# Performance work log

Hardware: AMD Instinct MI355X
Metric: run time of the kernel (lower is better)

The kernel has to match this reference:

```python
import jax, jax.numpy as jnp
import numpy as np

NE = 32          # n_events
S = 65536        # n_samples
FR = 128         # n_frames
SR = 22050       # samplerate
NRES = 1024      # n_resonances
IEXP = 8         # instr_expressivity
NEXP = 4         # noise_expressivity
NFILT = 64       # n_noise_filters
FSAMP = 512      # noise_filter_samples
NDEF = 64        # n_deformations
NNDEF = 32       # noise_deformations
NENV = 64        # n_envelopes
NDEC = 64        # n_decays
ENV_SMALL = 128  # Envelopes n_samples
ENV_FULL = 8192  # Envelopes full_size
NVERB = 16       # number of impulse responses


def interp_last(x, size):
    # linear interpolation along last axis (align_corners=True style)
    n = x.shape[-1]
    pos = jnp.linspace(0.0, n - 1.0, size)
    lo = jnp.floor(pos).astype(jnp.int32)
    hi = jnp.clip(lo + 1, 0, n - 1)
    w = (pos - lo).astype(x.dtype)
    return x[..., lo] * (1.0 - w) + x[..., hi] * w


def fft_convolve(a, b):
    # linear convolution via zero-padded FFT, keep first n samples
    n = a.shape[-1]
    A = jnp.fft.rfft(a, n=2 * n)
    B = jnp.fft.rfft(b, n=2 * n)
    return jnp.fft.irfft(A * B, n=2 * n)[..., :n]


def select_items(sel, items):
    # softmax-weighted soft lookup over item bank
    return jax.nn.softmax(sel, axis=-1) @ items


def make_waves(n_samples, n_res, sr):
    freqs = np.linspace(20.0, 4000.0, num=n_res // 4)
    t = np.arange(n_samples, dtype=np.float64) / sr
    ph = freqs[:, None] * t[None, :]               # cycles
    sine = np.sin(2 * np.pi * ph)
    saw = 2.0 * (ph % 1.0) - 1.0
    square = np.sign(sine)
    tri = 2.0 * np.abs(saw) - 1.0
    w = np.concatenate([sine, saw, square, tri], axis=0)  # (n_res, n_samples)
    return jnp.asarray(w, dtype=jnp.float32)


def setup_inputs() -> dict:
    key = jax.random.key(0)
    ks = jax.random.split(key, 16)
    u = lambda k, shp: jax.random.uniform(k, shp, minval=-0.02, maxval=0.02, dtype=jnp.float32)
    inp = {
        'res_sel': jax.random.normal(ks[0], (1, NE, IEXP, NRES), jnp.float32),
        'noise_sel': jax.random.normal(ks[1], (1, NE, NEXP, NFILT), jnp.float32),
        'env_sel': jax.random.normal(ks[2], (1, NE, NENV), jnp.float32),
        'dec_sel': jax.random.normal(ks[3], (1, NE, 1, NDEC), jnp.float32),
        'def_sel': jax.random.normal(ks[4], (1, NE, NDEF), jnp.float32),
        'noise_def_sel': jax.random.normal(ks[5], (1, NE, NNDEF), jnp.float32),
        'mix_sel': jax.random.normal(ks[6], (1, NE, 2), jnp.float32),
        'room_sel': jax.random.normal(ks[7], (1, NE, NVERB), jnp.float32),
        'amp': jax.random.uniform(ks[8], (1, NE, 1), dtype=jnp.float32),
        # learned item banks (uniform(-0.02, 0.02) init as in Lookup)
        'r_items': u(ks[9], (NRES, NRES)),
        'n_items': u(ks[10], (NFILT, FSAMP)),
        'e_items': u(ks[11], (NENV, ENV_SMALL)),
        'd_items': u(ks[12], (NDEC, 1)),
        'warp_items': u(ks[13], (NDEF, IEXP * FR)),
        'nwarp_items': u(ks[14], (NNDEF, NEXP * FR)),
        # fixed buffers
        'verbs': jax.random.normal(ks[15], (NVERB, S), jnp.float32) * 0.01,
        'waves': make_waves(S, NRES, SR),
    }
    return inp


def reference(res_sel, noise_sel, env_sel, dec_sel, def_sel, noise_def_sel,
              mix_sel, room_sel, amp, r_items, n_items, e_items, d_items,
              warp_items, nwarp_items, verbs, waves):
    # --- Envelopes: items**2, soft lookup, upsample, multiply by noise, pad ---
    env = select_items(env_sel, e_items ** 2)            # (1, NE, 128)
    env = interp_last(env, ENV_FULL)                     # (1, NE, 8192)
    noise = jax.random.uniform(jax.random.key(42), env.shape,
                               minval=-1.0, maxval=1.0, dtype=env.dtype)
    env = env * noise
    impulses = jnp.pad(env, ((0, 0), (0, 0), (0, S - ENV_FULL)))  # (1, NE, S)

    # --- SampleLookup (windowed noise filters) ---
    k = jnp.arange(FSAMP, dtype=jnp.float32)
    hamming = 0.54 - 0.46 * jnp.cos(2.0 * jnp.pi * k / (FSAMP - 1))
    nfil = select_items(noise_sel, n_items * hamming)    # (1, NE, NEXP, FSAMP)
    nfil = jnp.pad(nfil, ((0, 0), (0, 0), (0, 0), (0, S - FSAMP)))
    filt = fft_convolve(impulses[:, :, None, :], nfil)   # (1, NE, NEXP, S)

    # --- noise Deformations: softmax over channel dim, upsample ---
    nd = select_items(noise_def_sel, nwarp_items)        # (1, NE, NEXP*FR)
    nd = nd.reshape(1, NE, NEXP, FR)
    nd = jax.nn.softmax(nd, axis=2)
    nd = interp_last(nd, S)                              # (1, NE, NEXP, S)
    filtered = (filt * nd).sum(axis=2)                   # (1, NE, S)

    # --- WavetableLookup resonances ---
    res = select_items(res_sel, r_items) @ waves         # (1, NE, IEXP, S)

    # --- Decays: log-domain cumsum -> exponential envelopes ---
    d_pre = 0.5 + jax.nn.sigmoid(d_items) * 0.5          # base_resonance=0.5
    d = select_items(dec_sel, d_pre)                     # (1, NE, 1, 1)
    d = jnp.tile(d, (1, 1, 1, FR))                       # (1, NE, 1, FR)
    d = jnp.exp(jnp.cumsum(jnp.log(d + 1e-12), axis=-1))
    d = interp_last(d, S)                                # (1, NE, 1, S)

    # --- instrument Deformations ---
    w = select_items(def_sel, warp_items)                # (1, NE, IEXP*FR)
    w = w.reshape(1, NE, IEXP, FR)
    w = jax.nn.softmax(w, axis=2)
    w = interp_last(w, S)                                # (1, NE, IEXP, S)

    dres = (res * d * w).sum(axis=2)                     # (1, NE, S)

    # --- excite resonances with filtered noise, add reverb, mix ---
    conv = fft_convolve(filtered, dres)                  # (1, NE, S)
    rooms = select_items(room_sel, verbs)                # (1, NE, S)
    wet = fft_convolve(conv, rooms)
    m = jax.nn.softmax(mix_sel, axis=-1)                 # (1, NE, 2)
    mixed = m[..., 0:1] * conv + m[..., 1:2] * wet
    return mixed * (amp ** 2)                            # (1, NE, S)
```

## Files before the change

### kernel.cpp

```cpp
#include <hip/hip_runtime.h>
#include <math.h>

#define NEV    32
#define NS     65536
#define NFFT   131072
#define ENVS   128
#define ENVF   8192
#define FSAMP2 512
#define NEXP2  4
#define FLEN   8704
#define GD     5622750u
#define GDH    2811375u

enum : size_t {
  O_ENV_SMALL = 0,
  O_NFIL      = 4096,
  O_IMP       = 69632,
  O_ND        = 331776,
  O_WSM       = 348160,
  O_DSM       = 380928,
  O_SCAL      = 385024,
  O_RHO       = 385152,
  O_P1        = 385664,
  O_P2        = 647808,
// ... 73 lines not shown
  x0 += x1; x1 = tf_rotl(x1, 6); x1 ^= x0;
  x0 += k2; x1 += k0 + 5u;
  return x0 ^ x1;
}

__global__ __launch_bounds__(64) void weights_kernel(
    const float* __restrict__ noise_sel, const float* __restrict__ env_sel,
    const float* __restrict__ dec_sel,   const float* __restrict__ def_sel,
    const float* __restrict__ ndef_sel,  const float* __restrict__ mix_sel,
    const float* __restrict__ room_sel,  const float* __restrict__ amp,
    const float* __restrict__ d_items,
    float* __restrict__ swE, float* __restrict__ swN,
    float* __restrict__ swD, float* __restrict__ swND,
    float* __restrict__ d_small, float* __restrict__ scal,
    float* __restrict__ rho)
{
  const int e = blockIdx.x;
  const int l = threadIdx.x;

  {
    float x = env_sel[e*64 + l];
    float mx = wmax(x);
    float ex = expf(x - mx);
    float sm = wsum(ex);
    swE[e*64 + l] = ex / sm;
  }
  #pragma unroll
  for (int x4 = 0; x4 < NEXP2; x4++){
    float v = noise_sel[(e*NEXP2 + x4)*64 + l];
    float mxv = wmax(v);
    float exv = expf(v - mxv);
    float smv = wsum(exv);
    swN[(e*NEXP2 + x4)*64 + l] = exv / smv;
  }
  {
    float x = def_sel[e*64 + l];
    float mx = wmax(x);
    float ex = expf(x - mx);
    float sm = wsum(ex);
    swD[e*64 + l] = ex / sm;
  }
  {
    float x = (l < 32) ? ndef_sel[e*32 + l] : -1e30f;
    float mx = wmax(x);
    float ex = (l < 32) ? expf(x - mx) : 0.f;
    float sm = wsum(ex);
    if (l < 32) swND[e*32 + l] = ex / sm;
  }
  {
    float x = dec_sel[e*64 + l];
    float mx = wmax(x);
    float ex = expf(x - mx);
    float sm = wsum(ex);
    float wgt = ex / sm;
    float di = d_items[l];
    float dp = 0.5f + 0.5f*(1.0f/(1.0f + expf(-di)));
    float d0 = wsum(wgt*dp);
    float ld = logf(d0 + 1e-12f);
    #pragma unroll
    for (int c = 0; c < 2; c++){
      int f = l + 64*c;
      d_small[e*128 + f] = expf((float)(f+1)*ld);
    }
  }
  if (l == 0){
    float a = mix_sel[e*2 + 0], b = mix_sel[e*2 + 1];
    float mm = fmaxf(a, b);
    float ea = expf(a - mm), eb = expf(b - mm);
    float ss = ea + eb;
    scal[e*4 + 0] = ea/ss;
    scal[e*4 + 1] = eb/ss;
    float am = amp[e];
    scal[e*4 + 2] = am*am;
  }
  {
    float x = (l < 16) ? room_sel[e*16 + l] : -1e30f;
    float mx = wmax(x);
    float ex = (l < 16) ? expf(x - mx) : 0.f;
    float sm = wsum(ex);
    if (l < 16) rho[e*16 + l] = ex/sm;
  }
}

__global__ __launch_bounds__(128) void envs_kernel(
    const float* __restrict__ swE, const float* __restrict__ e_items,
    float* __restrict__ env_small)
{
  const int e = blockIdx.x, j = threadIdx.x;
  __shared__ float sw[64];
  if (j < 64) sw[j] = swE[e*64 + j];
  __syncthreads();
  float acc = 0.f;
  #pragma unroll 8
  for (int k = 0; k < 64; k++){ float it = e_items[k*ENVS + j]; acc += sw[k]*(it*it); }
  env_small[e*ENVS + j] = acc;
}

__global__ __launch_bounds__(256) void nfil_kernel(
    const float* __restrict__ swN, const float* __restrict__ n_items,
    float* __restrict__ nfil)
{
  const int b = blockIdx.x;
  const int tid = threadIdx.x;
  __shared__ float sw[64];
  if (tid < 64) sw[tid] = swN[b*64 + tid];
  __syncthreads();
  #pragma unroll
  for (int c = 0; c < 2; c++){
    int tau = tid + 256*c;
    float acc = 0.f;
    #pragma unroll 8
    for (int f = 0; f < 64; f++) acc += sw[f]*n_items[f*FSAMP2 + tau];
    float ham = 0.54f - 0.46f*cosf((6.2831853071795864769f * (float)tau) / 511.0f);
    nfil[b*FSAMP2 + tau] = acc*ham;
  }
}

__global__ __launch_bounds__(128) void warp_kernel(
    const float* __restrict__ swD, const float* __restrict__ warp_items,
    float* __restrict__ w_small)
{
  const int e = blockIdx.x, f = threadIdx.x;
  __shared__ float sw[64];
  if (f < 64) sw[f] = swD[e*64 + f];
  __syncthreads();
  float acc[8] = {0,0,0,0,0,0,0,0};
  for (int k = 0; k < 64; k++){
    float wk = sw[k];
    const float* row = warp_items + (size_t)k*1024 + f;
    #pragma unroll
    for (int i = 0; i < 8; i++) acc[i] += wk*row[i*128];
  }
  float mx = -1e30f;
  #pragma unroll
  for (int i = 0; i < 8; i++) mx = fmaxf(mx, acc[i]);
  float ev[8]; float s = 0.f;
  #pragma unroll
  for (int i = 0; i < 8; i++){ ev[i] = expf(acc[i] - mx); s += ev[i]; }
  #pragma unroll
  for (int i = 0; i < 8; i++) w_small[(e*8 + i)*128 + f] = ev[i]/s;
}

__global__ __launch_bounds__(128) void nwarp_kernel(
    const float* __restrict__ swND, const float* __restrict__ nwarp_items,
    float* __restrict__ nd_small)
{
  const int e = blockIdx.x, f = threadIdx.x;
  __shared__ float sw[32];
  if (f < 32) sw[f] = swND[e*32 + f];
  __syncthreads();
  float acc[4] = {0,0,0,0};
  for (int k = 0; k < 32; k++){
    float wk = sw[k];
    const float* row = nwarp_items + (size_t)k*512 + f;
    #pragma unroll
    for (int x = 0; x < 4; x++) acc[x] += wk*row[x*128];
  }
  float mx = -1e30f;
  #pragma unroll
  for (int x = 0; x < 4; x++) mx = fmaxf(mx, acc[x]);
  float ev[4]; float s = 0.f;
  #pragma unroll
  for (int x = 0; x < 4; x++){ ev[x] = expf(acc[x] - mx); s += ev[x]; }
  #pragma unroll
  for (int x = 0; x < 4; x++) nd_small[(e*4 + x)*128 + f] = ev[x]/s;
}

__global__ __launch_bounds__(64) void prep_kernel(
    const float* __restrict__ noise_sel, const float* __restrict__ env_sel,
    const float* __restrict__ dec_sel,   const float* __restrict__ def_sel,
    const float* __restrict__ ndef_sel,  const float* __restrict__ mix_sel,
    const float* __restrict__ room_sel,  const float* __restrict__ amp,
    const float* __restrict__ n_items,   const float* __restrict__ e_items,
    const float* __restrict__ d_items,   const float* __restrict__ warp_items,
    const float* __restrict__ nwarp_items,
    float* __restrict__ env_small, float* __restrict__ nfil,
    float* __restrict__ nd_small,  float* __restrict__ w_small,
    float* __restrict__ d_small,   float* __restrict__ scal,
    float* __restrict__ rho)
{
  const int e = blockIdx.x;
  const int l = threadIdx.x;
  __shared__ float sw[64];
  __shared__ float buf[1024];

  {
    float x = env_sel[e*64 + l];
    float mx = wmax(x);
    float ex = expf(x - mx);
    float sm = wsum(ex);
    sw[l] = ex / sm;
  }
  __syncthreads();
  #pragma unroll
  for (int c = 0; c < 2; c++){
    int j = l + 64*c;
    float acc = 0.f;
    for (int k = 0; k < 64; k++){ float it = e_items[k*ENVS + j]; acc += sw[k]*(it*it); }
    env_small[e*ENVS + j] = acc;
  }
  __syncthreads();

  for (int x = 0; x < NEXP2; x++){
    float v = noise_sel[(e*NEXP2 + x)*64 + l];
    float mxv = wmax(v);
    float exv = expf(v - mxv);
    float smv = wsum(exv);
    sw[l] = exv / smv;
    __syncthreads();
    for (int c = 0; c < 8; c++){
      int tau = l + 64*c;
      float acc = 0.f;
      for (int f = 0; f < 64; f++) acc += sw[f]*n_items[f*FSAMP2 + tau];
      float ham = 0.54f - 0.46f*cosf((6.2831853071795864769f * (float)tau) / 511.0f);
      nfil[(e*NEXP2 + x)*FSAMP2 + tau] = acc*ham;
    }
    __syncthreads();
  }

  {
    float x = def_sel[e*64 + l];
    float mx = wmax(x);
    float ex = expf(x - mx);
    float sm = wsum(ex);
    sw[l] = ex / sm;
  }
  __syncthreads();
  for (int c = 0; c < 16; c++){
    int idx = l + 64*c;
    float acc = 0.f;
    for (int k = 0; k < 64; k++) acc += sw[k]*warp_items[k*1024 + idx];
    buf[idx] = acc;
  }
  __syncthreads();
  #pragma unroll
  for (int c = 0; c < 2; c++){
    int f = l + 64*c;
    float mx = -1e30f;
    for (int i = 0; i < 8; i++) mx = fmaxf(mx, buf[i*128 + f]);
    float ev[8]; float s = 0.f;
    for (int i = 0; i < 8; i++){ ev[i] = expf(buf[i*128 + f] - mx); s += ev[i]; }
    for (int i = 0; i < 8; i++) w_small[(e*8 + i)*128 + f] = ev[i]/s;
  }
  __syncthreads();

  {
    float x = (l < 32) ? ndef_sel[e*32 + l] : -1e30f;
    float mx = wmax(x);
// ... 20 lines not shown
  }
  __syncthreads();

  {
    float x = dec_sel[e*64 + l];
    float mx = wmax(x);
    float ex = expf(x - mx);
    float sm = wsum(ex);
    float wgt = ex / sm;
    float di = d_items[l];
    float dp = 0.5f + 0.5f*(1.0f/(1.0f + expf(-di)));
    float d0 = wsum(wgt*dp);
    float ld = logf(d0 + 1e-12f);
    #pragma unroll
    for (int c = 0; c < 2; c++){
      int f = l + 64*c;
      d_small[e*128 + f] = expf((float)(f+1)*ld);
    }
  }
  if (l == 0){
    float a = mix_sel[e*2 + 0], b = mix_sel[e*2 + 1];
    float mm = fmaxf(a, b);
    float ea = expf(a - mm), eb = expf(b - mm);
    float ss = ea + eb;
    scal[e*4 + 0] = ea/ss;
    scal[e*4 + 1] = eb/ss;
    float am = amp[e];
    scal[e*4 + 2] = am*am;
  }
  {
    float x = (l < 16) ? room_sel[e*16 + l] : -1e30f;
    float mx = wmax(x);
    float ex = (l < 16) ? expf(x - mx) : 0.f;
    float sm = wsum(ex);
    if (l < 16) rho[e*16 + l] = ex/sm;
  }
}

__global__ __launch_bounds__(256) void p1_softmax_kernel(
    const float* __restrict__ res_sel, float* __restrict__ P1)
{
  const int m = blockIdx.x;
  const int tid = threadIdx.x;
  __shared__ float red[4], red2[4];
  const float* row = res_sel + (size_t)m*1024;
  float4 v = ((const float4*)row)[tid];
  float mx = fmaxf(fmaxf(v.x, v.y), fmaxf(v.z, v.w));
  #pragma unroll
  for (int o = 32; o > 0; o >>= 1) mx = fmaxf(mx, __shfl_xor(mx, o));
  if ((tid & 63) == 0) red[tid >> 6] = mx;
  __syncthreads();
  mx = fmaxf(fmaxf(red[0], red[1]), fmaxf(red[2], red[3]));
  float e0 = expf(v.x - mx), e1 = expf(v.y - mx), e2 = expf(v.z - mx), e3 = expf(v.w - mx);
  float s = e0 + e1 + e2 + e3;
  #pragma unroll
  for (int o = 32; o > 0; o >>= 1) s += __shfl_xor(s, o);
  if ((tid & 63) == 0) red2[tid >> 6] = s;
  __syncthreads();
  s = red2[0] + red2[1] + red2[2] + red2[3];
  float inv = 1.0f/s;
  ((float4*)(P1 + (size_t)m*1024))[tid] = make_float4(e0*inv, e1*inv, e2*inv, e3*inv);
}

__global__ __launch_bounds__(256) void p2_kernel(
    const float* __restrict__ P1, const float* __restrict__ r_items,
    float* __restrict__ P2)
{
  __shared__ __align__(16) float sp1[8][1024];
  const int bx = blockIdx.x;
  const int mg = blockIdx.y;
  const int tid = threadIdx.x;
  for (int idx = tid; idx < 2048; idx += 256)
    ((float4*)&sp1[0][0])[idx] = ((const float4*)(P1 + (size_t)mg*8*1024))[idx];
  __syncthreads();
  const int n = bx*256 + tid;
  float acc[8] = {0,0,0,0,0,0,0,0};
  for (int k = 0; k < 1024; k++){
    float wv = r_items[(size_t)k*1024 + n];
    #pragma unroll
    for (int r = 0; r < 8; r++) acc[r] += sp1[r][k]*wv;
  }
  #pragma unroll
  for (int r = 0; r < 8; r++) P2[(size_t)(mg*8 + r)*1024 + n] = acc[r];
}

__global__ __launch_bounds__(256) void split_a_kernel(
    const float* __restrict__ P2, unsigned short* __restrict__ Ahi)
{
  const int row = blockIdx.x;
  for (int k = threadIdx.x; k < 1024; k += 256){
    float f = P2[(size_t)row*1024 + k];
    Ahi[(size_t)(k >> 3)*2048 + row*8 + (k & 7)] = f2bf(f);
  }
}

__global__ __launch_bounds__(256) void env_noise_kernel(
    const float* __restrict__ env_small, float* __restrict__ impulses)
{
  const int flat = blockIdx.x*256 + threadIdx.x;
  const int e = flat >> 13, i = flat & 8191;
  unsigned bits = threefry_bits(0u, (unsigned)flat);
  float u01 = __uint_as_float((bits >> 9) | 0x3f800000u) - 1.0f;
  float nz  = fmaxf(-1.0f, u01*2.0f - 1.0f);
  float pos = (float)i * (127.0f/8191.0f);
  int lo = (int)floorf(pos);
  int hi = imin(lo + 1, 127);
  float w = pos - (float)lo;
  const float* es = env_small + e*ENVS;
  float v = es[lo]*(1.0f - w) + es[hi]*w;
  impulses[flat] = v*nz;
}

__global__ __launch_bounds__(256) void filt_kernel(
    const float* __restrict__ nfil, const float* __restrict__ impulses,
    const float* __restrict__ nd_small, float* __restrict__ filtered)
{
  __shared__ float nf[4*512];
  __shared__ float imp[768];
  const int e = blockIdx.y, t0 = blockIdx.x*256, tid = threadIdx.x;
  for (int idx = tid; idx < 2048; idx += 256) nf[idx] = nfil[e*2048 + idx];
  for (int idx = tid; idx < 768; idx += 256){
    int g = t0 - 512 + idx;
    imp[idx] = (g >= 0 && g < ENVF) ? impulses[e*ENVF + g] : 0.f;
  }
  __syncthreads();
  const int t = t0 + tid;
  float s0 = 0.f, s1 = 0.f, s2 = 0.f, s3 = 0.f;
  for (int tau = 0; tau < 512; tau++){
    float iv = imp[512 + tid - tau];
    s0 += nf[0*512 + tau]*iv;
    s1 += nf[1*512 + tau]*iv;
    s2 += nf[2*512 + tau]*iv;
    s3 += nf[3*512 + tau]*iv;
  }
  float pos = (float)t * (127.0f/65535.0f);
  int lo = (int)floorf(pos);
  int hi = imin(lo + 1, 127);
  float w = pos - (float)lo;
  const float* nds = nd_small + e*512;
  float acc = 0.f;
  acc += s0*(nds[0*128 + lo]*(1.0f - w) + nds[0*128 + hi]*w);
  acc += s1*(nds[1*128 + lo]*(1.0f - w) + nds[1*128 + hi]*w);
  acc += s2*(nds[2*128 + lo]*(1.0f - w) + nds[2*128 + hi]*w);
  acc += s3*(nds[3*128 + lo]*(1.0f - w) + nds[3*128 + hi]*w);
  filtered[e*FLEN + t] = acc;
}

__global__ __launch_bounds__(256) void rooms_kernel(
    const float* __restrict__ verbs, const float* __restrict__ rho,
    float* __restrict__ rooms)
{
  const int t = blockIdx.x*256 + threadIdx.x;
  const int e = blockIdx.y;
  float acc = 0.f;
  #pragma unroll
  for (int v = 0; v < 16; v++) acc += rho[e*16 + v]*verbs[(size_t)v*NS + t];
  rooms[(size_t)e*NS + t] = acc;
}

__device__ __noinline__ float slow_wave(int wf, int n, int i){
  const double stp = 3980.0 / 255.0;
  double fi = (i == 255) ? 4000.0 : __dadd_rn(__dmul_rn((double)i, stp), 20.0);
  double tn = (double)n / 22050.0;
  double ph = __dmul_rn(fi, tn);
  double fr = ph - trunc(ph);
  if (wf == 1) return (float)(2.0*fr - 1.0);
  if (wf == 3){ double sw = 2.0*fr - 1.0; return (float)(2.0*fabs(sw) - 1.0); }
  if (fr == 0.0 || fr == 0.5){
    if (ph == 0.0) return 0.0f;
    double sv = sin(__dmul_rn(6.283185307179586, ph));
    return (sv > 0.0) ? 1.0f : ((sv < 0.0) ? -1.0f : 0.0f);
  }
  return (fr < 0.5) ? 1.0f : -1.0f;
}

__device__ __forceinline__ void gen8(int wf, int n, int i0,
// ... 198 lines not shown
                                         float* __restrict__ yi)
{
  const int tid = threadIdx.x;
  constexpr int BPR = L/4;
  #pragma unroll
  for (int q = 0; q < 4; q++){
    int bf = tid + 256*q;
    int r  = bf / BPR;
    int j  = bf % BPR;
    int sw = (r & 7) << 2;
    int jm = j & (Ns - 1);
    float2 w1 = twid((float)jm * (1.0f/(4.0f*(float)Ns)));
    if (DIR < 0) w1.y = -w1.y;
    float2 w2 = make_float2(w1.x*w1.x - w1.y*w1.y, 2.0f*w1.x*w1.y);
    float2 w3 = make_float2(w2.x*w1.x - w2.y*w1.y, w2.x*w1.y + w2.y*w1.x);
    const float* xrr = xr + r*L;
    const float* xir = xi + r*L;
    float ar  = xrr[j ^ sw],           ai  = xir[j ^ sw];
    float b0r = xrr[(j+BPR) ^ sw],     b0i = xir[(j+BPR) ^ sw];
    float c0r = xrr[(j+2*BPR) ^ sw],   c0i = xir[(j+2*BPR) ^ sw];
    float d0r = xrr[(j+3*BPR) ^ sw],   d0i = xir[(j+3*BPR) ^ sw];
    float br = b0r*w1.x - b0i*w1.y,  bi = b0r*w1.y + b0i*w1.x;
    float cr = c0r*w2.x - c0i*w2.y,  ci = c0r*w2.y + c0i*w2.x;
    float dr = d0r*w3.x - d0i*w3.y,  di = d0r*w3.y + d0i*w3.x;
    float apc_r = ar + cr, apc_i = ai + ci;
    float amc_r = ar - cr, amc_i = ai - ci;
    float bpd_r = br + dr, bpd_i = bi + di;
    float bmd_r = br - dr, bmd_i = bi - di;
    int dbase = ((j - jm) << 2) + jm;
    float* yrr = yr + r*L;
    float* yir = yi + r*L;
    yrr[dbase ^ sw]          = apc_r + bpd_r;
    yir[dbase ^ sw]          = apc_i + bpd_i;
    yrr[(dbase + 2*Ns) ^ sw] = apc_r - bpd_r;
    yir[(dbase + 2*Ns) ^ sw] = apc_i - bpd_i;
    if (DIR > 0){
      yrr[(dbase + Ns) ^ sw]   = amc_r + bmd_i;
      yir[(dbase + Ns) ^ sw]   = amc_i - bmd_r;
      yrr[(dbase + 3*Ns) ^ sw] = amc_r - bmd_i;
      yir[(dbase + 3*Ns) ^ sw] = amc_i + bmd_r;
    } else {
      yrr[(dbase + Ns) ^ sw]   = amc_r - bmd_i;
      yir[(dbase + Ns) ^ sw]   = amc_i + bmd_r;
      yrr[(dbase + 3*Ns) ^ sw] = amc_r + bmd_i;
      yir[(dbase + 3*Ns) ^ sw] = amc_i - bmd_r;
    }
  }
}

#define FFT_SWAP { float* t_; t_=ra;ra=rb;rb=t_; t_=ia;ia=ib;ib=t_; }

template<int L, int DIR>
__device__ __forceinline__ void fft_core4(float*& ra, float*& ia, float*& rb, float*& ib)
{
  const int tid = threadIdx.x;
  if (L == 512){
    __syncthreads();
    #pragma unroll
    for (int q = 0; q < 8; q++){
      int bf = tid + 256*q;
      int r = bf >> 8, j = bf & 255;
      int sw = (r & 7) << 2;
      float ar = ra[r*512 + (j ^ sw)],        ai = ia[r*512 + (j ^ sw)];
      float br = ra[r*512 + ((j+256) ^ sw)],  bi = ia[r*512 + ((j+256) ^ sw)];
      rb[r*512 + ((2*j) ^ sw)]   = ar + br;
      ib[r*512 + ((2*j) ^ sw)]   = ai + bi;
      rb[r*512 + ((2*j+1) ^ sw)] = ar - br;
      ib[r*512 + ((2*j+1) ^ sw)] = ai - bi;
    }
    FFT_SWAP
    __syncthreads(); r4_stage<512,   2, DIR>(ra, ia, rb, ib); FFT_SWAP
    __syncthreads(); r4_stage<512,   8, DIR>(ra, ia, rb, ib); FFT_SWAP
    __syncthreads(); r4_stage<512,  32, DIR>(ra, ia, rb, ib); FFT_SWAP
    __syncthreads(); r4_stage<512, 128, DIR>(ra, ia, rb, ib); FFT_SWAP
  } else {
    __syncthreads(); r4_stage<256,   1, DIR>(ra, ia, rb, ib); FFT_SWAP
    __syncthreads(); r4_stage<256,   4, DIR>(ra, ia, rb, ib); FFT_SWAP
    __syncthreads(); r4_stage<256,  16, DIR>(ra, ia, rb, ib); FFT_SWAP
    __syncthreads(); r4_stage<256,  64, DIR>(ra, ia, rb, ib); FFT_SWAP
  }
  __syncthreads();
}

__global__ __launch_bounds__(256) void fwd512_pack_kernel(
    const float* __restrict__ srcA, int lenA, int strideA,
    const float* __restrict__ srcB, int lenB, int strideB,
    float2* __restrict__ Bt)
{
  __shared__ float reA[4096], imA[4096], reB[4096], imB[4096];
  const int e = blockIdx.y, t1 = blockIdx.x*8, tid = threadIdx.x;
  #pragma unroll
  for (int q = 0; q < 4; q++){
    int flat = tid + 256*q;
    int n2 = flat >> 1;
    int rb = (flat & 1)*4;
    int nb = t1 + rb + 256*n2;
    float4 va = make_float4(0.f,0.f,0.f,0.f);
    float4 vb = make_float4(0.f,0.f,0.f,0.f);
    if (nb < lenA) va = *(const float4*)(srcA + (size_t)e*strideA + nb);
    if (nb < lenB) vb = *(const float4*)(srcB + (size_t)e*strideB + nb);
    #pragma unroll
    for (int j = 0; j < 4; j++){
      int r = rb + j;
      int sw = (r & 7) << 2;
      reA[r*512 + (n2 ^ sw)] = (&va.x)[j];
      imA[r*512 + (n2 ^ sw)] = (&vb.x)[j];
    }
  }
  float *ra = reA, *ia = imA, *rb2 = reB, *ib2 = imB;
  fft_core4<512, +1>(ra, ia, rb2, ib2);
  float2* dst = Bt + ((size_t)e << 17);
  #pragma unroll
  for (int q = 0; q < 16; q++){
    int idx = tid + 256*q;
    int r = idx & 7, k2 = idx >> 3;
    int n1 = t1 + r;
    int sw = (r & 7) << 2;
    float xr = ra[r*512 + (k2 ^ sw)];
    float xi = ia[r*512 + (k2 ^ sw)];
    float2 w = twid((float)(n1*k2) * (1.0f/131072.0f));
    dst[k2*256 + n1] = make_float2(xr*w.x - xi*w.y, xr*w.y + xi*w.x);
  }
}

__global__ __launch_bounds__(256) void fwd512_pack_rooms_kernel(
    const float* __restrict__ verbs, const float* __restrict__ rho,
    float2* __restrict__ Bt)
{
  __shared__ float reA[4096], imA[4096], reB[4096], imB[4096];
  __shared__ float srho[32];
  const int e = blockIdx.y, t1 = blockIdx.x*8, tid = threadIdx.x;
  if (tid < 32) srho[tid] = rho[(2*e)*16 + tid];
  __syncthreads();
  #pragma unroll
  for (int q = 0; q < 4; q++){
    int flat = tid + 256*q;
    int n2 = flat >> 1;
    int rb = (flat & 1)*4;
    int nb = t1 + rb + 256*n2;
    float4 va = make_float4(0.f,0.f,0.f,0.f);
    float4 vb = make_float4(0.f,0.f,0.f,0.f);
    if (nb < NS){
      #pragma unroll
      for (int v = 0; v < 16; v++){
        float4 w4 = *(const float4*)(verbs + (size_t)v*NS + nb);
        float r0 = srho[v], r1 = srho[16 + v];
        va.x += r0*w4.x; va.y += r0*w4.y; va.z += r0*w4.z; va.w += r0*w4.w;
        vb.x += r1*w4.x; vb.y += r1*w4.y; vb.z += r1*w4.z; vb.w += r1*w4.w;
      }
    }
    #pragma unroll
    for (int j = 0; j < 4; j++){
      int r = rb + j;
      int sw = (r & 7) << 2;
      reA[r*512 + (n2 ^ sw)] = (&va.x)[j];
      imA[r*512 + (n2 ^ sw)] = (&vb.x)[j];
    }
  }
  float *ra = reA, *ia = imA, *rb2 = reB, *ib2 = imB;
  fft_core4<512, +1>(ra, ia, rb2, ib2);
  float2* dst = Bt + ((size_t)e << 17);
  #pragma unroll
  for (int q = 0; q < 16; q++){
    int idx = tid + 256*q;
    int r = idx & 7, k2 = idx >> 3;
    int n1 = t1 + r;
    int sw = (r & 7) << 2;
    float xr = ra[r*512 + (k2 ^ sw)];
    float xi = ia[r*512 + (k2 ^ sw)];
    float2 w = twid((float)(n1*k2) * (1.0f/131072.0f));
    dst[k2*256 + n1] = make_float2(xr*w.x - xi*w.y, xr*w.y + xi*w.x);
  }
}

__global__ __launch_bounds__(256) void fwd256_kernel(float2* __restrict__ S)
{
  __shared__ float reA[4096], imA[4096], reB[4096], imB[4096];
  const int e = blockIdx.y, K0 = blockIdx.x*16, tid = threadIdx.x;
  float2* base = S + ((size_t)e << 17) + (size_t)K0*256;
  #pragma unroll
  for (int q = 0; q < 16; q++){
    int idx = tid + 256*q;
    int r = idx >> 8, col = idx & 255;
    float2 v = base[r*256 + col];
    int sw = (r & 7) << 2;
    reA[r*256 + (col ^ sw)] = v.x;
    imA[r*256 + (col ^ sw)] = v.y;
  }
  float *ra = reA, *ia = imA, *rb = reB, *ib = imB;
  fft_core4<256, +1>(ra, ia, rb, ib);
  #pragma unroll
  for (int q = 0; q < 16; q++){
    int idx = tid + 256*q;
    int r = idx >> 8, col = idx & 255;
    int sw = (r & 7) << 2;
    base[r*256 + col] = make_float2(ra[r*256 + (col ^ sw)], ia[r*256 + (col ^ sw)]);
  }
}

__global__ __launch_bounds__(256) void inv256_mul2_kernel(
    const float2* __restrict__ ZA, const float2* __restrict__ ZB,
    float2* __restrict__ Ut)
{
  __shared__ float reA[4096], imA[4096], reB[4096], imB[4096];
  const int e = blockIdx.y, K0 = blockIdx.x*16, tid = threadIdx.x;
  const float2* Za = ZA + ((size_t)e << 17);
  const float2* Zb = ZB + ((size_t)e << 17);
  #pragma unroll
  for (int q = 0; q < 16; q++){
    int idx = tid + 256*q;
    int r = idx >> 8, col = idx & 255;
    int k2 = K0 + r;
    int k2p, k1p;
    if (k2 == 0){ k2p = 0; k1p = (256 - col) & 255; }
    else        { k2p = 512 - k2; k1p = 255 - col; }
    float2 za  = Za[(size_t)k2*256 + col];
    float2 zap = Za[(size_t)k2p*256 + k1p];
    float2 zb  = Zb[(size_t)k2*256 + col];
    float2 zbp = Zb[(size_t)k2p*256 + k1p];
    float a0r = 0.5f*(za.x + zap.x), a0i = 0.5f*(za.y - zap.y);
    float a1r = 0.5f*(za.y + zap.y), a1i = 0.5f*(zap.x - za.x);
    float b0r = 0.5f*(zb.x + zbp.x), b0i = 0.5f*(zb.y - zbp.y);
    float b1r = 0.5f*(zb.y + zbp.y), b1i = 0.5f*(zbp.x - zb.x);
    float p0r = a0r*b0r - a0i*b0i, p0i = a0r*b0i + a0i*b0r;
    float p1r = a1r*b1r - a1i*b1i, p1i = a1r*b1i + a1i*b1r;
    int sw = (r & 7) << 2;
    reA[r*256 + (col ^ sw)] = p0r - p1i;
    imA[r*256 + (col ^ sw)] = p0i + p1r;
  }
  float *ra = reA, *ia = imA, *rb = reB, *ib = imB;
  fft_core4<256, -1>(ra, ia, rb, ib);
  float2* dst = Ut + ((size_t)e << 17);
  #pragma unroll
  for (int q = 0; q < 16; q++){
    int idx = tid + 256*q;
    int r = idx & 15, n1 = idx >> 4;
    int k2 = K0 + r;
    int sw = (r & 7) << 2;
    float xr = ra[r*256 + (n1 ^ sw)];
    float xi = ia[r*256 + (n1 ^ sw)];
    float2 w = twid((float)(n1*k2) * (1.0f/131072.0f));
    dst[n1*512 + k2] = make_float2(xr*w.x + xi*w.y, xi*w.x - xr*w.y);
  }
}

__global__ __launch_bounds__(256) void inv512_fwdpack2_kernel(
    const float2* __restrict__ Ut, float* __restrict__ conv,
    float2* __restrict__ Bt)
{
  __shared__ float reA[4096], imA[4096], reB[4096], imB[4096];
  const int e = blockIdx.y, t1 = blockIdx.x*8, tid = threadIdx.x;
  const float2* base = Ut + ((size_t)e << 17) + (size_t)t1*512;
  #pragma unroll
  for (int q = 0; q < 16; q++){
    int idx = tid + 256*q;
    int r = idx >> 9, col = idx & 511;
    float2 v = base[r*512 + col];
    int sw = (r & 7) << 2;
    reA[r*512 + (col ^ sw)] = v.x;
    imA[r*512 + (col ^ sw)] = v.y;
  }
  float *ra = reA, *ia = imA, *rb = reB, *ib = imB;
  fft_core4<512, -1>(ra, ia, rb, ib);
  const float s = 1.0f/131072.0f;
  #pragma unroll
  for (int q = 0; q < 16; q++){
    int idx = tid + 256*q;
    int r = idx & 7, n2 = idx >> 3;
    int sw = (r & 7) << 2;
    int pos = r*512 + (n2 ^ sw);
    if (n2 < 256){
      int n = (t1 + r) + 256*n2;
      float y0 = ra[pos]*s, y1 = ia[pos]*s;
      conv[(size_t)(2*e)*NS + n]     = y0;
      conv[(size_t)(2*e + 1)*NS + n] = y1;
      rb[pos] = y0; ib[pos] = y1;
    } else {
      rb[pos] = 0.f; ib[pos] = 0.f;
    }
  }
// ... 61 lines not shown
  const int e = blockIdx.y;
  const int t0 = blockIdx.x * 2048;
  const int tid = threadIdx.x;
  const int tb = tid * 8;
  float acc[8] = {0,0,0,0,0,0,0,0};
  const int kcap = imin(sig_len, t0 + 2048);
  for (int c0 = 0; c0 < kcap; c0 += 2048){
    __syncthreads();
    for (int idx = tid; idx < 2048; idx += 256){
      int gsi = c0 + idx;
      cs[idx] = (gsi < sig_len) ? sig[(size_t)e*sig_stride + gsi] : 0.f;
    }
    const int rb = t0 - c0 - 2056;
    for (int idx = tid; idx < 4104; idx += 256){
      int g = rb + idx;
      rs[idx] = (g >= 0 && g < NS) ? go[(size_t)e*NS + g] : 0.f;
    }
    __syncthreads();
    float W[12];
    int P = tb + 2056;
    *(float4*)&W[0] = *(const float4*)&rs[P - 4];
    *(float4*)&W[4] = *(const float4*)&rs[P];
    *(float4*)&W[8] = *(const float4*)&rs[P + 4];
    for (int u = 0; u < 512; u++){
      float4 f4 = *(const float4*)&cs[4*u];
      #pragma unroll
      for (int j = 0; j < 8; j++){
        acc[j] += f4.x*W[4 + j];
        acc[j] += f4.y*W[3 + j];
        acc[j] += f4.z*W[2 + j];
        acc[j] += f4.w*W[1 + j];
      }
      #pragma unroll
      for (int x2 = 11; x2 >= 4; x2--) W[x2] = W[x2 - 4];
      P -= 4;
      *(float4*)&W[0] = *(const float4*)&rs[P - 4];
    }
  }
  if (MODE == 0){
    #pragma unroll
    for (int j = 0; j < 8; j++) dst[(size_t)e*NS + t0 + tb + j] = acc[j];
  } else {
    float m0 = scal[e*4 + 0], m1 = scal[e*4 + 1], a2 = scal[e*4 + 2];
    #pragma unroll
    for (int j = 0; j < 8; j++){
      size_t gi = (size_t)e*NS + t0 + tb + j;
      dst[gi] = (m0*sig[gi] + m1*acc[j]) * a2;
    }
  }
}

extern "C" void kernel_launch(void* const* d_in, const int* in_sizes, int n_in,
                              void* d_out, int out_size, void* d_ws, size_t ws_size,
                              hipStream_t stream)
{
  (void)in_sizes; (void)n_in; (void)out_size;
  const float* res_sel     = (const float*)d_in[0];
  const float* noise_sel   = (const float*)d_in[1];
  const float* env_sel     = (const float*)d_in[2];
  const float* dec_sel     = (const float*)d_in[3];
  const float* def_sel     = (const float*)d_in[4];
  const float* ndef_sel    = (const float*)d_in[5];
  const float* mix_sel     = (const float*)d_in[6];
  const float* room_sel    = (const float*)d_in[7];
  const float* amp         = (const float*)d_in[8];
  const float* r_items     = (const float*)d_in[9];
  const float* n_items     = (const float*)d_in[10];
  const float* e_items     = (const float*)d_in[11];
  const float* d_items     = (const float*)d_in[12];
  const float* warp_items  = (const float*)d_in[13];
  const float* nwarp_items = (const float*)d_in[14];
  const float* verbs       = (const float*)d_in[15];
  const float* waves       = (const float*)d_in[16];
  float* ws  = (float*)d_ws;
  float* out = (float*)d_out;

  const bool big_ws = ws_size >= (size_t)O_END * sizeof(float);

  if (big_ws) {
    weights_kernel<<<dim3(NEV), dim3(64), 0, stream>>>(
        noise_sel, env_sel, dec_sel, def_sel, ndef_sel, mix_sel, room_sel, amp,
        d_items, ws + O_SWE, ws + O_SWN, ws + O_SWD, ws + O_SWND,
        ws + O_DSM, ws + O_SCAL, ws + O_RHO);
    envs_kernel<<<dim3(NEV), dim3(128), 0, stream>>>(ws + O_SWE, e_items, ws + O_ENV_SMALL);
    nfil_kernel<<<dim3(128), dim3(256), 0, stream>>>(ws + O_SWN, n_items, ws + O_NFIL);
    warp_kernel<<<dim3(NEV), dim3(128), 0, stream>>>(ws + O_SWD, warp_items, ws + O_WSM);
    nwarp_kernel<<<dim3(NEV), dim3(128), 0, stream>>>(ws + O_SWND, nwarp_items, ws + O_ND);

    p1_softmax_kernel<<<dim3(256), dim3(256), 0, stream>>>(res_sel, ws + O_P1);
    p2_kernel<<<dim3(4, 32), dim3(256), 0, stream>>>(ws + O_P1, r_items, ws + O_P2);

    env_noise_kernel<<<dim3(1024), dim3(256), 0, stream>>>(ws + O_ENV_SMALL, ws + O_IMP);
    filt_kernel<<<dim3(34, NEV), dim3(256), 0, stream>>>(ws + O_NFIL, ws + O_IMP, ws + O_ND, ws + O_FILT);

    unsigned short* Ahi = (unsigned short*)(ws + O_X);
    split_a_kernel<<<dim3(256), dim3(256), 0, stream>>>(ws + O_P2, Ahi);
    gemm_dres_gen3_kernel<<<dim3(512), dim3(512), 0, stream>>>(
        Ahi, ws + O_WSM, ws + O_DSM, ws + O_DRES);

    float2* Xf = (float2*)(ws + O_X);
    float2* Xd = (float2*)(ws + O_X + 4194304);
    float2* Xr = (float2*)(ws + O_Y);
    float2* Uc = (float2*)(ws + O_Y + 4194304);
    float2* Xc = Xf;
    float2* Uw = Xd;

    fwd512_pack_kernel<<<dim3(32, 16), dim3(256), 0, stream>>>(
        ws + O_FILT, FLEN, 2*FLEN, ws + O_FILT + FLEN, FLEN, 2*FLEN, Xf);
    fwd256_kernel<<<dim3(32, 16), dim3(256), 0, stream>>>(Xf);
    fwd512_pack_kernel<<<dim3(32, 16), dim3(256), 0, stream>>>(
        ws + O_DRES, NS, 2*NS, ws + O_DRES + NS, NS, 2*NS, Xd);
    fwd256_kernel<<<dim3(32, 16), dim3(256), 0, stream>>>(Xd);
    fwd512_pack_rooms_kernel<<<dim3(32, 16), dim3(256), 0, stream>>>(
        verbs, ws + O_RHO, Xr);
    fwd256_kernel<<<dim3(32, 16), dim3(256), 0, stream>>>(Xr);

    inv256_mul2_kernel<<<dim3(32, 16), dim3(256), 0, stream>>>(Xf, Xd, Uc);
    inv512_fwdpack2_kernel<<<dim3(32, 16), dim3(256), 0, stream>>>(Uc, ws + O_CONV, Xc);
    fwd256_kernel<<<dim3(32, 16), dim3(256), 0, stream>>>(Xc);
    inv256_mul2_kernel<<<dim3(32, 16), dim3(256), 0, stream>>>(Xc, Xr, Uw);
    inv512_mix2_kernel<<<dim3(32, 16), dim3(256), 0, stream>>>(
        Uw, ws + O_CONV, ws + O_SCAL, out);
  } else {
    prep_kernel<<<dim3(NEV), dim3(64), 0, stream>>>(
        noise_sel, env_sel, dec_sel, def_sel, ndef_sel, mix_sel, room_sel, amp,
        n_items, e_items, d_items, warp_items, nwarp_items,
        ws + O_ENV_SMALL, ws + O_NFIL, ws + O_ND, ws + O_WSM,
        ws + O_DSM, ws + O_SCAL, ws + O_RHO);
    p1_softmax_kernel<<<dim3(256), dim3(256), 0, stream>>>(res_sel, ws + O_P1);
    p2_kernel<<<dim3(4, 32), dim3(256), 0, stream>>>(ws + O_P1, r_items, ws + O_P2);
    env_noise_kernel<<<dim3(1024), dim3(256), 0, stream>>>(ws + O_ENV_SMALL, ws + O_IMP);
    filt_kernel<<<dim3(34, NEV), dim3(256), 0, stream>>>(ws + O_NFIL, ws + O_IMP, ws + O_ND, ws + O_FILT);
    rooms_kernel<<<dim3(256, NEV), dim3(256), 0, stream>>>(verbs, ws + O_RHO, ws + O_ROOMS);
    gemm_dres_kernel<<<dim3(1024), dim3(256), 0, stream>>>(
        ws + O_P2, waves, ws + O_WSM, ws + O_DSM, ws + O_DRES);
    tconv_kernel<0><<<dim3(32, NEV), dim3(256), 0, stream>>>(
        ws + O_FILT, FLEN, FLEN, ws + O_DRES, (const float*)nullptr, ws + O_CONV);
    tconv_kernel<1><<<dim3(32, NEV), dim3(256), 0, stream>>>(
        ws + O_CONV, NS, NS, ws + O_ROOMS, ws + O_SCAL, out);
  }
}
```

Measured before the change: 388.2 us.

## Merge lookup kernels, fuse softmax and bf16 split into p2, batch forward FFTs

Four small lookup kernels become one launch that dispatches on block index. The res_sel softmax and the bf16 scatter are folded into the P2 matmul kernel, which removes two launches and the P1/P2 round trips through global memory. The three forward 512-point pack FFTs and the three 256-point passes each become one launch with a z-dimension, giving more blocks per launch and fewer launch gaps. In exchange, the softmax is now recomputed redundantly by each of the 4 x-blocks, and the fused kernels have more divergent code paths.

```diff
diff --git a/kernel.cpp b/kernel.cpp
--- a/kernel.cpp
+++ b/kernel.cpp
@@ -179,88 +179,126 @@
   }
 }
 
-__global__ __launch_bounds__(128) void envs_kernel(
-    const float* __restrict__ swE, const float* __restrict__ e_items,
-    float* __restrict__ env_small)
-{
-  const int e = blockIdx.x, j = threadIdx.x;
+__global__ __launch_bounds__(256) void lookups_kernel(
+    const float* __restrict__ swE,  const float* __restrict__ swN,
+    const float* __restrict__ swD,  const float* __restrict__ swND,
+    const float* __restrict__ e_items, const float* __restrict__ n_items,
+    const float* __restrict__ warp_items, const float* __restrict__ nwarp_items,
+    float* __restrict__ env_small, float* __restrict__ nfil,
+    float* __restrict__ w_small,   float* __restrict__ nd_small)
+{
   __shared__ float sw[64];
-  if (j < 64) sw[j] = swE[e*64 + j];
-  __syncthreads();
-  float acc = 0.f;
-  #pragma unroll 8
-  for (int k = 0; k < 64; k++){ float it = e_items[k*ENVS + j]; acc += sw[k]*(it*it); }
-  env_small[e*ENVS + j] = acc;
-}
-
-__global__ __launch_bounds__(256) void nfil_kernel(
-    const float* __restrict__ swN, const float* __restrict__ n_items,
-    float* __restrict__ nfil)
-{
   const int b = blockIdx.x;
   const int tid = threadIdx.x;
-  __shared__ float sw[64];
-  if (tid < 64) sw[tid] = swN[b*64 + tid];
-  __syncthreads();
-  #pragma unroll
-  for (int c = 0; c < 2; c++){
-    int tau = tid + 256*c;
-    float acc = 0.f;
+
+  if (b < 32){
+    const int e = b, j = tid;
+    if (j < 64) sw[j] = swE[e*64 + j];
+    __syncthreads();
+    if (j < 128){
+      float acc = 0.f;
+      #pragma unroll 8
+      for (int k = 0; k < 64; k++){ float it = e_items[k*ENVS + j]; acc += sw[k]*(it*it); }
+      env_small[e*ENVS + j] = acc;
+    }
+  } else if (b < 160){
+    const int bb = b - 32;
+    if (tid < 64) sw[tid] = swN[bb*64 + tid];
+    __syncthreads();
+    #pragma unroll
+    for (int c = 0; c < 2; c++){
+      int tau = tid + 256*c;
+      float acc = 0.f;
+      #pragma unroll 8
+      for (int f = 0; f < 64; f++) acc += sw[f]*n_items[f*FSAMP2 + tau];
+      float ham = 0.54f - 0.46f*cosf((6.2831853071795864769f * (float)tau) / 511.0f);
+      nfil[bb*FSAMP2 + tau] = acc*ham;
+    }
+  } else if (b < 192){
+    const int e = b - 160, f = tid;
+    if (f < 64) sw[f] = swD[e*64 + f];
+    __syncthreads();
+    if (f < 128){
+      float acc[8] = {0,0,0,0,0,0,0,0};
+      for (int k = 0; k < 64; k++){
+        float wk = sw[k];
+        const float* row = warp_items + (size_t)k*1024 + f;
+        #pragma unroll
+        for (int i = 0; i < 8; i++) acc[i] += wk*row[i*128];
+      }
+      float mx = -1e30f;
+      #pragma unroll
+      for (int i = 0; i < 8; i++) mx = fmaxf(mx, acc[i]);
+      float ev[8]; float s = 0.f;
+      #pragma unroll
+      for (int i = 0; i < 8; i++){ ev[i] = expf(acc[i] - mx); s += ev[i]; }
+      #pragma unroll
+      for (int i = 0; i < 8; i++) w_small[(e*8 + i)*128 + f] = ev[i]/s;
+    }
+  } else {
+    const int e = b - 192, f = tid;
+    if (f < 32) sw[f] = swND[e*32 + f];
+    __syncthreads();
+    if (f < 128){
+      float acc[4] = {0,0,0,0};
+      for (int k = 0; k < 32; k++){
+        float wk = sw[k];
+        const float* row = nwarp_items + (size_t)k*512 + f;
+        #pragma unroll
+        for (int x = 0; x < 4; x++) acc[x] += wk*row[x*128];
+      }
+      float mx = -1e30f;
+      #pragma unroll
+      for (int x = 0; x < 4; x++) mx = fmaxf(mx, acc[x]);
+      float ev[4]; float s = 0.f;
+      #pragma unroll
+      for (int x = 0; x < 4; x++){ ev[x] = expf(acc[x] - mx); s += ev[x]; }
+      #pragma unroll
+      for (int x = 0; x < 4; x++) nd_small[(e*4 + x)*128 + f] = ev[x]/s;
+    }
+  }
+}
+
+__global__ __launch_bounds__(256) void p2s_kernel(
+    const float* __restrict__ res_sel, const float* __restrict__ r_items,
+    unsigned short* __restrict__ Ahi)
+{
+  __shared__ __align__(16) float sp1[8][1024];
+  const int bx = blockIdx.x;
+  const int mg = blockIdx.y;
+  const int tid = threadIdx.x;
+  for (int idx = tid; idx < 2048; idx += 256)
+    ((float4*)&sp1[0][0])[idx] = ((const float4*)(res_sel + (size_t)mg*8*1024))[idx];
+  __syncthreads();
+  {
+    const int r = tid >> 5, lr = tid & 31;
+    float mx = -1e30f;
     #pragma unroll 8
-    for (int f = 0; f < 64; f++) acc += sw[f]*n_items[f*FSAMP2 + tau];
-    float ham = 0.54f - 0.46f*cosf((6.2831853071795864769f * (float)tau) / 511.0f);
-    nfil[b*FSAMP2 + tau] = acc*ham;
-  }
-}
-
-__global__ __launch_bounds__(128) void warp_kernel(
-    const float* __restrict__ swD, const float* __restrict__ warp_items,
-    float* __restrict__ w_small)
-{
-  const int e = blockIdx.x, f = threadIdx.x;
-  __shared__ float sw[64];
-  if (f < 64) sw[f] = swD[e*64 + f];
-  __syncthreads();
+    for (int k = 0; k < 32; k++) mx = fmaxf(mx, sp1[r][lr + 32*k]);
+    #pragma unroll
+    for (int o = 16; o > 0; o >>= 1) mx = fmaxf(mx, __shfl_xor(mx, o));
+    float sm = 0.f;
+    float ev[32];
+    #pragma unroll 8
+    for (int k = 0; k < 32; k++){ ev[k] = expf(sp1[r][lr + 32*k] - mx); sm += ev[k]; }
+    #pragma unroll
+    for (int o = 16; o > 0; o >>= 1) sm += __shfl_xor(sm, o);
+    float inv = 1.0f/sm;
+    #pragma unroll 8
+    for (int k = 0; k < 32; k++) sp1[r][lr + 32*k] = ev[k]*inv;
+  }
+  __syncthreads();
+  const int n = bx*256 + tid;
   float acc[8] = {0,0,0,0,0,0,0,0};
-  for (int k = 0; k < 64; k++){
-    float wk = sw[k];
-    const float* row = warp_items + (size_t)k*1024 + f;
-    #pragma unroll
-    for (int i = 0; i < 8; i++) acc[i] += wk*row[i*128];
-  }
-  float mx = -1e30f;
-  #pragma unroll
-  for (int i = 0; i < 8; i++) mx = fmaxf(mx, acc[i]);
-  float ev[8]; float s = 0.f;
-  #pragma unroll
-  for (int i = 0; i < 8; i++){ ev[i] = expf(acc[i] - mx); s += ev[i]; }
-  #pragma unroll
-  for (int i = 0; i < 8; i++) w_small[(e*8 + i)*128 + f] = ev[i]/s;
-}
-
-__global__ __launch_bounds__(128) void nwarp_kernel(
-    const float* __restrict__ swND, const float* __restrict__ nwarp_items,
-    float* __restrict__ nd_small)
-{
-  const int e = blockIdx.x, f = threadIdx.x;
-  __shared__ float sw[32];
-  if (f < 32) sw[f] = swND[e*32 + f];
-  __syncthreads();
-  float acc[4] = {0,0,0,0};
-  for (int k = 0; k < 32; k++){
-    float wk = sw[k];
-    const float* row = nwarp_items + (size_t)k*512 + f;
-    #pragma unroll
-    for (int x = 0; x < 4; x++) acc[x] += wk*row[x*128];
-  }
-  float mx = -1e30f;
-  #pragma unroll
-  for (int x = 0; x < 4; x++) mx = fmaxf(mx, acc[x]);
-  float ev[4]; float s = 0.f;
-  #pragma unroll
-  for (int x = 0; x < 4; x++){ ev[x] = expf(acc[x] - mx); s += ev[x]; }
-  #pragma unroll
-  for (int x = 0; x < 4; x++) nd_small[(e*4 + x)*128 + f] = ev[x]/s;
+  for (int k = 0; k < 1024; k++){
+    float wv = r_items[(size_t)k*1024 + n];
+    #pragma unroll
+    for (int r = 0; r < 8; r++) acc[r] += sp1[r][k]*wv;
+  }
+  const size_t base = (size_t)(n >> 3)*2048 + (size_t)(n & 7);
+  #pragma unroll
+  for (int r = 0; r < 8; r++)
+    Ahi[base + (size_t)(mg*8 + r)*8] = f2bf(acc[r]);
 }
 
 __global__ __launch_bounds__(64) void prep_kernel(
@@ -447,16 +485,6 @@
   }
   #pragma unroll
   for (int r = 0; r < 8; r++) P2[(size_t)(mg*8 + r)*1024 + n] = acc[r];
-}
-
-__global__ __launch_bounds__(256) void split_a_kernel(
-    const float* __restrict__ P2, unsigned short* __restrict__ Ahi)
-{
-  const int row = blockIdx.x;
-  for (int k = threadIdx.x; k < 1024; k += 256){
-    float f = P2[(size_t)row*1024 + k];
-    Ahi[(size_t)(k >> 3)*2048 + row*8 + (k & 7)] = f2bf(f);
-  }
 }
 
 __global__ __launch_bounds__(256) void env_noise_kernel(
@@ -821,13 +849,19 @@
   __syncthreads();
 }
 
-__global__ __launch_bounds__(256) void fwd512_pack_kernel(
-    const float* __restrict__ srcA, int lenA, int strideA,
-    const float* __restrict__ srcB, int lenB, int strideB,
-    float2* __restrict__ Bt)
+__global__ __launch_bounds__(256) void fwd512_all_kernel(
+    const float* __restrict__ filt, const float* __restrict__ dresv,
+    const float* __restrict__ verbs, const float* __restrict__ rho,
+    float2* __restrict__ Xf, float2* __restrict__ Xd, float2* __restrict__ Xr)
 {
   __shared__ float reA[4096], imA[4096], reB[4096], imB[4096];
+  __shared__ float srho[32];
   const int e = blockIdx.y, t1 = blockIdx.x*8, tid = threadIdx.x;
+  const int z = blockIdx.z;
+  if (z == 2){
+    if (tid < 32) srho[tid] = rho[(2*e)*16 + tid];
+    __syncthreads();
+  }
   #pragma unroll
   for (int q = 0; q < 4; q++){
     int flat = tid + 256*q;
@@ -836,8 +870,27 @@
     int nb = t1 + rb + 256*n2;
     float4 va = make_float4(0.f,0.f,0.f,0.f);
     float4 vb = make_float4(0.f,0.f,0.f,0.f);
-    if (nb < lenA) va = *(const float4*)(srcA + (size_t)e*strideA + nb);
-    if (nb < lenB) vb = *(const float4*)(srcB + (size_t)e*strideB + nb);
+    if (z == 0){
+      if (nb < FLEN){
+        va = *(const float4*)(filt + (size_t)e*2*FLEN + nb);
+        vb = *(const float4*)(filt + (size_t)e*2*FLEN + FLEN + nb);
+      }
+    } else if (z == 1){
+      if (nb < NS){
+        va = *(const float4*)(dresv + (size_t)e*2*NS + nb);
+        vb = *(const float4*)(dresv + (size_t)e*2*NS + NS + nb);
+      }
+    } else {
+      if (nb < NS){
+        #pragma unroll
+        for (int v = 0; v < 16; v++){
+          float4 w4 = *(const float4*)(verbs + (size_t)v*NS + nb);
+          float r0 = srho[v], r1 = srho[16 + v];
+          va.x += r0*w4.x; va.y += r0*w4.y; va.z += r0*w4.z; va.w += r0*w4.w;
+          vb.x += r1*w4.x; vb.y += r1*w4.y; vb.z += r1*w4.z; vb.w += r1*w4.w;
+        }
+      }
+    }
     #pragma unroll
     for (int j = 0; j < 4; j++){
       int r = rb + j;
@@ -848,6 +901,7 @@
   }
   float *ra = reA, *ia = imA, *rb2 = reB, *ib2 = imB;
   fft_core4<512, +1>(ra, ia, rb2, ib2);
+  float2* Bt = (z == 0) ? Xf : (z == 1) ? Xd : Xr;
   float2* dst = Bt + ((size_t)e << 17);
   #pragma unroll
   for (int q = 0; q < 16; q++){
@@ -862,57 +916,7 @@
   }
 }
 
-__global__ __launch_bounds__(256) void fwd512_pack_rooms_kernel(
-    const float* __restrict__ verbs, const float* __restrict__ rho,
-    float2* __restrict__ Bt)
-{
-  __shared__ float reA[4096], imA[4096], reB[4096], imB[4096];
-  __shared__ float srho[32];
-  const int e = blockIdx.y, t1 = blockIdx.x*8, tid = threadIdx.x;
-  if (tid < 32) srho[tid] = rho[(2*e)*16 + tid];
-  __syncthreads();
-  #pragma unroll
-  for (int q = 0; q < 4; q++){
-    int flat = tid + 256*q;
-    int n2 = flat >> 1;
-    int rb = (flat & 1)*4;
-    int nb = t1 + rb + 256*n2;
-    float4 va = make_float4(0.f,0.f,0.f,0.f);
-    float4 vb = make_float4(0.f,0.f,0.f,0.f);
-    if (nb < NS){
-      #pragma unroll
-      for (int v = 0; v < 16; v++){
-        float4 w4 = *(const float4*)(verbs + (size_t)v*NS + nb);
-        float r0 = srho[v], r1 = srho[16 + v];
-        va.x += r0*w4.x; va.y += r0*w4.y; va.z += r0*w4.z; va.w += r0*w4.w;
-        vb.x += r1*w4.x; vb.y += r1*w4.y; vb.z += r1*w4.z; vb.w += r1*w4.w;
-      }
-    }
-    #pragma unroll
-    for (int j = 0; j < 4; j++){
-      int r = rb + j;
-      int sw = (r & 7) << 2;
-      reA[r*512 + (n2 ^ sw)] = (&va.x)[j];
-      imA[r*512 + (n2 ^ sw)] = (&vb.x)[j];
-    }
-  }
-  float *ra = reA, *ia = imA, *rb2 = reB, *ib2 = imB;
-  fft_core4<512, +1>(ra, ia, rb2, ib2);
-  float2* dst = Bt + ((size_t)e << 17);
-  #pragma unroll
-  for (int q = 0; q < 16; q++){
-    int idx = tid + 256*q;
-    int r = idx & 7, k2 = idx >> 3;
-    int n1 = t1 + r;
-    int sw = (r & 7) << 2;
-    float xr = ra[r*512 + (k2 ^ sw)];
-    float xi = ia[r*512 + (k2 ^ sw)];
-    float2 w = twid((float)(n1*k2) * (1.0f/131072.0f));
-    dst[k2*256 + n1] = make_float2(xr*w.x - xi*w.y, xr*w.y + xi*w.x);
-  }
-}
-
-__global__ __launch_bounds__(256) void fwd256_kernel(float2* __restrict__ S)
+__device__ __forceinline__ void fwd256_body(float2* __restrict__ S)
 {
   __shared__ float reA[4096], imA[4096], reB[4096], imB[4096];
   const int e = blockIdx.y, K0 = blockIdx.x*16, tid = threadIdx.x;
@@ -935,6 +939,18 @@
     int sw = (r & 7) << 2;
     base[r*256 + col] = make_float2(ra[r*256 + (col ^ sw)], ia[r*256 + (col ^ sw)]);
   }
+}
+
+__global__ __launch_bounds__(256) void fwd256_tri_kernel(
+    float2* __restrict__ Xf, float2* __restrict__ Xd, float2* __restrict__ Xr)
+{
+  float2* S = (blockIdx.z == 0) ? Xf : (blockIdx.z == 1) ? Xd : Xr;
+  fwd256_body(S);
+}
+
+__global__ __launch_bounds__(256) void fwd256_kernel(float2* __restrict__ S)
+{
+  fwd256_body(S);
 }
 
 __global__ __launch_bounds__(256) void inv256_mul2_kernel(
@@ -1162,19 +1178,17 @@
         noise_sel, env_sel, dec_sel, def_sel, ndef_sel, mix_sel, room_sel, amp,
         d_items, ws + O_SWE, ws + O_SWN, ws + O_SWD, ws + O_SWND,
         ws + O_DSM, ws + O_SCAL, ws + O_RHO);
-    envs_kernel<<<dim3(NEV), dim3(128), 0, stream>>>(ws + O_SWE, e_items, ws + O_ENV_SMALL);
-    nfil_kernel<<<dim3(128), dim3(256), 0, stream>>>(ws + O_SWN, n_items, ws + O_NFIL);
-    warp_kernel<<<dim3(NEV), dim3(128), 0, stream>>>(ws + O_SWD, warp_items, ws + O_WSM);
-    nwarp_kernel<<<dim3(NEV), dim3(128), 0, stream>>>(ws + O_SWND, nwarp_items, ws + O_ND);
-
-    p1_softmax_kernel<<<dim3(256), dim3(256), 0, stream>>>(res_sel, ws + O_P1);
-    p2_kernel<<<dim3(4, 32), dim3(256), 0, stream>>>(ws + O_P1, r_items, ws + O_P2);
+    lookups_kernel<<<dim3(224), dim3(256), 0, stream>>>(
+        ws + O_SWE, ws + O_SWN, ws + O_SWD, ws + O_SWND,
+        e_items, n_items, warp_items, nwarp_items,
+        ws + O_ENV_SMALL, ws + O_NFIL, ws + O_WSM, ws + O_ND);
+
+    unsigned short* Ahi = (unsigned short*)(ws + O_X);
+    p2s_kernel<<<dim3(4, 32), dim3(256), 0, stream>>>(res_sel, r_items, Ahi);
 
     env_noise_kernel<<<dim3(1024), dim3(256), 0, stream>>>(ws + O_ENV_SMALL, ws + O_IMP);
     filt_kernel<<<dim3(34, NEV), dim3(256), 0, stream>>>(ws + O_NFIL, ws + O_IMP, ws + O_ND, ws + O_FILT);
 
-    unsigned short* Ahi = (unsigned short*)(ws + O_X);
-    split_a_kernel<<<dim3(256), dim3(256), 0, stream>>>(ws + O_P2, Ahi);
     gemm_dres_gen3_kernel<<<dim3(512), dim3(512), 0, stream>>>(
         Ahi, ws + O_WSM, ws + O_DSM, ws + O_DRES);
 
@@ -1185,15 +1199,9 @@
     float2* Xc = Xf;
     float2* Uw = Xd;
 
-    fwd512_pack_kernel<<<dim3(32, 16), dim3(256), 0, stream>>>(
-        ws + O_FILT, FLEN, 2*FLEN, ws + O_FILT + FLEN, FLEN, 2*FLEN, Xf);
-    fwd256_kernel<<<dim3(32, 16), dim3(256), 0, stream>>>(Xf);
-    fwd512_pack_kernel<<<dim3(32, 16), dim3(256), 0, stream>>>(
-        ws + O_DRES, NS, 2*NS, ws + O_DRES + NS, NS, 2*NS, Xd);
-    fwd256_kernel<<<dim3(32, 16), dim3(256), 0, stream>>>(Xd);
-    fwd512_pack_rooms_kernel<<<dim3(32, 16), dim3(256), 0, stream>>>(
-        verbs, ws + O_RHO, Xr);
-    fwd256_kernel<<<dim3(32, 16), dim3(256), 0, stream>>>(Xr);
+    fwd512_all_kernel<<<dim3(32, 16, 3), dim3(256), 0, stream>>>(
+        ws + O_FILT, ws + O_DRES, verbs, ws + O_RHO, Xf, Xd, Xr);
+    fwd256_tri_kernel<<<dim3(32, 16, 3), dim3(256), 0, stream>>>(Xf, Xd, Xr);
 
     inv256_mul2_kernel<<<dim3(32, 16), dim3(256), 0, stream>>>(Xf, Xd, Uc);
     inv512_fwdpack2_kernel<<<dim3(32, 16), dim3(256), 0, stream>>>(Uc, ws + O_CONV, Xc);
```

New measurement: 356.2 us. -8.2%, faster.
